# Optimization experiments

Hardware: AMD Instinct MI355X
Metric: run time of the kernel (lower is better)

The kernel has to match this reference:

```python
import jax, jax.numpy as jnp
import numpy as np

BS, NCAM, N, S = 2, 3, 64, 256


def setup_inputs() -> dict:
    key = jax.random.key(0)
    ks = jax.random.split(key, 7)
    # 2D projected points in pixel coordinates [0, image_size)
    points = jax.random.uniform(ks[0], (BS, NCAM, N, 2), dtype=jnp.float32) * S
    # blob params (per-point), realistic trained-model ranges
    sigmas = jax.random.uniform(ks[1], (BS, N), dtype=jnp.float32) * 0.05 + 0.02
    exponents = jax.random.uniform(ks[2], (BS, N), dtype=jnp.float32) * 0.5 + 0.75
    intensities = jax.random.uniform(ks[3], (BS, N), dtype=jnp.float32) * 0.5 + 0.5
    # per-camera scale factors, near 1
    camera_sigmas = jax.random.uniform(ks[4], (BS, NCAM), dtype=jnp.float32) * 0.2 + 0.9
    camera_exponents = jax.random.uniform(ks[5], (BS, NCAM), dtype=jnp.float32) * 0.2 + 0.9
    camera_intensities = jax.random.uniform(ks[6], (BS, NCAM), dtype=jnp.float32) * 0.2 + 0.9
    return {
        "points": points,
        "sigmas": sigmas,
        "exponents": exponents,
        "intensities": intensities,
        "camera_sigmas": camera_sigmas,
        "camera_exponents": camera_exponents,
        "camera_intensities": camera_intensities,
        "image_size": S,
    }


def reference(points, sigmas, exponents, intensities,
              camera_sigmas, camera_exponents, camera_intensities, image_size):
    """Faithful JAX port of render_points (render_mode='gaussians')."""
    bs, ncam, n = points.shape[0], points.shape[1], points.shape[2]
    s2 = image_size // 2
    # normalize pixel coords to [-1, 1] and flatten batch*cameras
    p = jnp.clip((points - s2) / s2, -1.0, 1.0).reshape(bs * ncam, n, 2)
    # per-point params scaled by per-camera factors; repeat_interleave(3,0)
    # on (bs,N) == broadcast over camera axis then flatten -> (bs*3, N, 1, 1)
    sig = (sigmas[:, None, :] * camera_sigmas[:, :, None]).reshape(bs * ncam, n, 1, 1)
    expn = (exponents[:, None, :] * camera_exponents[:, :, None]).reshape(bs * ncam, n, 1, 1)
    inten = (intensities[:, None, :] * camera_intensities[:, :, None]).reshape(bs * ncam, n, 1, 1)
    grid = jnp.linspace(-1.0, 1.0, image_size, dtype=jnp.float32)
    # m[y, x] = (grid[x], grid[y]); squared distance to each point
    dx = grid[None, None, None, :] - p[:, :, 0, None, None]   # (bs*3, N, 1, W)
    dy = grid[None, None, :, None] - p[:, :, 1, None, None]   # (bs*3, N, H, 1)
    dst = dx * dx + dy * dy                                   # (bs*3, N, H, W)
    blobs = jnp.exp(-((dst / (2.0 * sig * sig)) ** expn))      # (bs*3, N, H, W)
    masks = jnp.minimum(jnp.max(blobs * inten, axis=1), 1.0)   # amax over N, clamp(max=1)
    masks = masks.reshape(bs, ncam, image_size, image_size)
    blobs = blobs.reshape(bs, ncam, n, image_size, image_size)
    return masks, blobs
```

## Files before the change

kernel.cpp:

```cpp
#include <hip/hip_runtime.h>
#include <hip/hip_bf16.h>

constexpr int S_IMG = 256;
constexpr int NPT   = 64;
constexpr int BC    = 6;
constexpr int NCAM_ = 3;

__global__ __launch_bounds__(256) void render_blobs_kernel(
    const float* __restrict__ points,
    const float* __restrict__ sigmas,
    const float* __restrict__ exponents,
    const float* __restrict__ intensities,
    const float* __restrict__ cam_sig,
    const float* __restrict__ cam_exp,
    const float* __restrict__ cam_int,
    float* __restrict__ masks,
    float* __restrict__ blobs)
{
    const int blk = blockIdx.x;
    const int bc  = blk >> 7;
    const int y0  = (blk & 127) << 1;
    const int b   = bc / NCAM_;
    const int t   = threadIdx.x;

    __shared__ float spx[NPT], spy[NPT], sk[NPT], se[NPT], si[NPT];
    if (t < NPT) {
        const float inv = 1.0f / 128.0f;
        float px = points[(bc * NPT + t) * 2 + 0];
        float py = points[(bc * NPT + t) * 2 + 1];
        px = fminf(fmaxf((px - 128.0f) * inv, -1.0f), 1.0f);
        py = fminf(fmaxf((py - 128.0f) * inv, -1.0f), 1.0f);
        float sg = sigmas[b * NPT + t] * cam_sig[bc];
        spx[t] = px;
        spy[t] = py;
        sk[t]  = 1.0f / (2.0f * sg * sg);
        se[t]  = exponents[b * NPT + t] * cam_exp[bc];
        si[t]  = intensities[b * NPT + t] * cam_int[bc];
    }
    __syncthreads();

    const int lin = t << 1;
    const int y   = y0 + (lin >> 8);
    const int x   = lin & 255;

    const float step = 2.0f / 255.0f;
    const float gx0  = fmaf((float)x, step, -1.0f);
    const float gx1  = gx0 + step;
    const float gy   = fmaf((float)y, step, -1.0f);

    float m0 = 0.0f, m1 = 0.0f;
    float* bp = blobs + (size_t)bc * NPT * S_IMG * S_IMG + (size_t)y * S_IMG + x;
    const size_t nstride = (size_t)S_IMG * S_IMG;

    #pragma unroll 4
    for (int n = 0; n < NPT; ++n) {
        float dx0 = gx0 - spx[n];
        float dx1 = gx1 - spx[n];
        float dy  = gy  - spy[n];
        float dy2 = dy * dy;
        float u0  = fmaf(dx0, dx0, dy2) * sk[n];
        float u1  = fmaf(dx1, dx1, dy2) * sk[n];
        float e   = se[n];
        float v0 = exp2f(e * __log2f(u0));
        float v1 = exp2f(e * __log2f(u1));
        float b0 = exp2f(-1.4426950408889634f * v0);
        float b1 = exp2f(-1.4426950408889634f * v1);
        *reinterpret_cast<float2*>(bp + n * nstride) = make_float2(b0, b1);
        float it = si[n];
        m0 = fmaxf(m0, b0 * it);
        m1 = fmaxf(m1, b1 * it);
    }

    float2 mm = make_float2(fminf(m0, 1.0f), fminf(m1, 1.0f));
    *reinterpret_cast<float2*>(masks + (size_t)bc * S_IMG * S_IMG + (size_t)y * S_IMG + x) = mm;
}

extern "C" void kernel_launch(void* const* d_in, const int* in_sizes, int n_in,
                              void* d_out, int out_size, void* d_ws, size_t ws_size,
                              hipStream_t stream) {
    const float* points      = (const float*)d_in[0];
    const float* sigmas      = (const float*)d_in[1];
    const float* exponents   = (const float*)d_in[2];
    const float* intensities = (const float*)d_in[3];
    const float* cam_sig     = (const float*)d_in[4];
    const float* cam_exp     = (const float*)d_in[5];
    const float* cam_int     = (const float*)d_in[6];

    float* masks = (float*)d_out;
    float* blobs = (float*)d_out + (size_t)BC * S_IMG * S_IMG;

    dim3 grid(BC * (S_IMG / 2));
    dim3 block(256);
    render_blobs_kernel<<<grid, block, 0, stream>>>(
        points, sigmas, exponents, intensities, cam_sig, cam_exp, cam_int,
        masks, blobs);
}
```

Before: 24.26 us.

## Split blob writes and mask reduction into separate block roles with vec4 nontemporal stores

Blocks are split into two roles. Blob blocks each write one point's full 256x256 plane, so their float4 stores are contiguous and nontemporal. Separate mask blocks recompute all 64 blobs per pixel to take the max. This replaces the old scheme of 2-wide stores strided across 64 planes and aims to raise write efficiency on the dominant ~100MB blob output. The cost is that the mask path does a second full evaluation of the transcendental work.

```diff
diff --git a/kernel.cpp b/kernel.cpp
--- a/kernel.cpp
+++ b/kernel.cpp
@@ -1,12 +1,21 @@
 #include <hip/hip_runtime.h>
-#include <hip/hip_bf16.h>
 
 constexpr int S_IMG = 256;
 constexpr int NPT   = 64;
 constexpr int BC    = 6;
 constexpr int NCAM_ = 3;
+constexpr int NBLOB_BLOCKS = BC * NPT;
+constexpr int NMASK_BLOCKS = BC * (S_IMG / 2);
 
-__global__ __launch_bounds__(256) void render_blobs_kernel(
+typedef float vf4 __attribute__((ext_vector_type(4)));
+typedef float vf2 __attribute__((ext_vector_type(2)));
+
+__device__ __forceinline__ float blob_eval(float u, float e) {
+    float v = exp2f(e * __log2f(u));
+    return exp2f(-1.4426950408889634f * v);
+}
+
+__global__ __launch_bounds__(256) void render_all(
     const float* __restrict__ points,
     const float* __restrict__ sigmas,
     const float* __restrict__ exponents,
@@ -17,62 +26,100 @@
     float* __restrict__ masks,
     float* __restrict__ blobs)
 {
-    const int blk = blockIdx.x;
-    const int bc  = blk >> 7;
-    const int y0  = (blk & 127) << 1;
-    const int b   = bc / NCAM_;
-    const int t   = threadIdx.x;
+    const int   blk  = blockIdx.x;
+    const int   t    = threadIdx.x;
+    const float step = 2.0f / 255.0f;
 
-    __shared__ float spx[NPT], spy[NPT], sk[NPT], se[NPT], si[NPT];
-    if (t < NPT) {
-        const float inv = 1.0f / 128.0f;
-        float px = points[(bc * NPT + t) * 2 + 0];
-        float py = points[(bc * NPT + t) * 2 + 1];
-        px = fminf(fmaxf((px - 128.0f) * inv, -1.0f), 1.0f);
-        py = fminf(fmaxf((py - 128.0f) * inv, -1.0f), 1.0f);
-        float sg = sigmas[b * NPT + t] * cam_sig[bc];
-        spx[t] = px;
-        spy[t] = py;
-        sk[t]  = 1.0f / (2.0f * sg * sg);
-        se[t]  = exponents[b * NPT + t] * cam_exp[bc];
-        si[t]  = intensities[b * NPT + t] * cam_int[bc];
+    if (blk < NBLOB_BLOCKS) {
+        const int bc = blk >> 6;
+        const int n  = blk & 63;
+        const int b  = bc / NCAM_;
+
+        float px = points[blk * 2 + 0];
+        float py = points[blk * 2 + 1];
+        px = fminf(fmaxf((px - 128.0f) * (1.0f / 128.0f), -1.0f), 1.0f);
+        py = fminf(fmaxf((py - 128.0f) * (1.0f / 128.0f), -1.0f), 1.0f);
+        float sg = sigmas[b * NPT + n] * cam_sig[bc];
+        float k  = 1.0f / (2.0f * sg * sg);
+        float e  = exponents[b * NPT + n] * cam_exp[bc];
+
+        float* bp = blobs + ((size_t)blk << 16);
+
+        const int x0 = (t & 63) << 2;
+        const int ty = t >> 6;
+
+        float kdx2[4];
+        #pragma unroll
+        for (int j = 0; j < 4; ++j) {
+            float gx = fmaf((float)(x0 + j), step, -1.0f);
+            float dx = gx - px;
+            kdx2[j] = k * dx * dx;
+        }
+
+        #pragma unroll 2
+        for (int it = 0; it < 64; ++it) {
+            const int y  = (it << 2) | ty;
+            float gy  = fmaf((float)y, step, -1.0f);
+            float dyv = gy - py;
+            float kdy2 = k * dyv * dyv;
+            vf4 o;
+            o.x = blob_eval(kdx2[0] + kdy2, e);
+            o.y = blob_eval(kdx2[1] + kdy2, e);
+            o.z = blob_eval(kdx2[2] + kdy2, e);
+            o.w = blob_eval(kdx2[3] + kdy2, e);
+            __builtin_nontemporal_store(o, (vf4*)(bp + ((size_t)y << 8) + x0));
+        }
+    } else {
+        const int blk2 = blk - NBLOB_BLOCKS;
+        const int bc   = blk2 >> 7;
+        const int y0   = (blk2 & 127) << 1;
+        const int b    = bc / NCAM_;
+
+        __shared__ float spx[NPT], spy[NPT], sk[NPT], se[NPT], si[NPT];
+        if (t < NPT) {
+            float px = points[(bc * NPT + t) * 2 + 0];
+            float py = points[(bc * NPT + t) * 2 + 1];
+            px = fminf(fmaxf((px - 128.0f) * (1.0f / 128.0f), -1.0f), 1.0f);
+            py = fminf(fmaxf((py - 128.0f) * (1.0f / 128.0f), -1.0f), 1.0f);
+            float sg = sigmas[b * NPT + t] * cam_sig[bc];
+            spx[t] = px;
+            spy[t] = py;
+            sk[t]  = 1.0f / (2.0f * sg * sg);
+            se[t]  = exponents[b * NPT + t] * cam_exp[bc];
+            si[t]  = intensities[b * NPT + t] * cam_int[bc];
+        }
+        __syncthreads();
+
+        const int lin = t << 1;
+        const int y   = y0 + (lin >> 8);
+        const int x   = lin & 255;
+
+        const float gx0 = fmaf((float)x, step, -1.0f);
+        const float gx1 = gx0 + step;
+        const float gy  = fmaf((float)y, step, -1.0f);
+
+        float m0 = 0.0f, m1 = 0.0f;
+        #pragma unroll 4
+        for (int n = 0; n < NPT; ++n) {
+            float kk  = sk[n];
+            float dx0 = gx0 - spx[n];
+            float dx1 = gx1 - spx[n];
+            float dyv = gy  - spy[n];
+            float kdy2 = kk * dyv * dyv;
+            float e   = se[n];
+            float b0  = blob_eval(fmaf(kk * dx0, dx0, kdy2), e);
+            float b1  = blob_eval(fmaf(kk * dx1, dx1, kdy2), e);
+            float it  = si[n];
+            m0 = fmaxf(m0, b0 * it);
+            m1 = fmaxf(m1, b1 * it);
+        }
+
+        vf2 mm;
+        mm.x = fminf(m0, 1.0f);
+        mm.y = fminf(m1, 1.0f);
+        __builtin_nontemporal_store(
+            mm, (vf2*)(masks + ((size_t)bc << 16) + ((size_t)y << 8) + x));
     }
-    __syncthreads();
-
-    const int lin = t << 1;
-    const int y   = y0 + (lin >> 8);
-    const int x   = lin & 255;
-
-    const float step = 2.0f / 255.0f;
-    const float gx0  = fmaf((float)x, step, -1.0f);
-    const float gx1  = gx0 + step;
-    const float gy   = fmaf((float)y, step, -1.0f);
-
-    float m0 = 0.0f, m1 = 0.0f;
-    float* bp = blobs + (size_t)bc * NPT * S_IMG * S_IMG + (size_t)y * S_IMG + x;
-    const size_t nstride = (size_t)S_IMG * S_IMG;
-
-    #pragma unroll 4
-    for (int n = 0; n < NPT; ++n) {
-        float dx0 = gx0 - spx[n];
-        float dx1 = gx1 - spx[n];
-        float dy  = gy  - spy[n];
-        float dy2 = dy * dy;
-        float u0  = fmaf(dx0, dx0, dy2) * sk[n];
-        float u1  = fmaf(dx1, dx1, dy2) * sk[n];
-        float e   = se[n];
-        float v0 = exp2f(e * __log2f(u0));
-        float v1 = exp2f(e * __log2f(u1));
-        float b0 = exp2f(-1.4426950408889634f * v0);
-        float b1 = exp2f(-1.4426950408889634f * v1);
-        *reinterpret_cast<float2*>(bp + n * nstride) = make_float2(b0, b1);
-        float it = si[n];
-        m0 = fmaxf(m0, b0 * it);
-        m1 = fmaxf(m1, b1 * it);
-    }
-
-    float2 mm = make_float2(fminf(m0, 1.0f), fminf(m1, 1.0f));
-    *reinterpret_cast<float2*>(masks + (size_t)bc * S_IMG * S_IMG + (size_t)y * S_IMG + x) = mm;
 }
 
 extern "C" void kernel_launch(void* const* d_in, const int* in_sizes, int n_in,
@@ -89,9 +136,9 @@
     float* masks = (float*)d_out;
     float* blobs = (float*)d_out + (size_t)BC * S_IMG * S_IMG;
 
-    dim3 grid(BC * (S_IMG / 2));
+    dim3 grid(NBLOB_BLOCKS + NMASK_BLOCKS);
     dim3 block(256);
-    render_blobs_kernel<<<grid, block, 0, stream>>>(
+    render_all<<<grid, block, 0, stream>>>(
         points, sigmas, exponents, intensities, cam_sig, cam_exp, cam_int,
         masks, blobs);
 }
```

Measured after the change: 38.64 us. +59.3%, slower.

## Split point loop across two blocks and combine masks with atomicMax

Applied to the files above, without the earlier changes.

Each block now handles half of the 64 points for a pair of rows, so the grid doubles and each thread runs a shorter loop. Partial mask maxima are combined through integer atomicMax on the float bits, which is valid because the values are non-negative, after a memset zeroes the mask buffer. This adds parallelism and shortens per-thread latency, at the cost of an extra memset operation on the stream and atomic traffic on the masks. The distance computation is also refactored slightly, folding the scale factor into the fma.

```diff
diff --git a/kernel.cpp b/kernel.cpp
--- a/kernel.cpp
+++ b/kernel.cpp
@@ -1,12 +1,19 @@
 #include <hip/hip_runtime.h>
-#include <hip/hip_bf16.h>
 
 constexpr int S_IMG = 256;
 constexpr int NPT   = 64;
 constexpr int BC    = 6;
 constexpr int NCAM_ = 3;
+constexpr int NHALF = 32;
 
-__global__ __launch_bounds__(256) void render_blobs_kernel(
+typedef float vf2 __attribute__((ext_vector_type(2)));
+
+__device__ __forceinline__ float blob_eval(float u, float e) {
+    float v = exp2f(e * __log2f(u));
+    return exp2f(-1.4426950408889634f * v);
+}
+
+__global__ __launch_bounds__(256) void render_fused(
     const float* __restrict__ points,
     const float* __restrict__ sigmas,
     const float* __restrict__ exponents,
@@ -17,25 +24,27 @@
     float* __restrict__ masks,
     float* __restrict__ blobs)
 {
-    const int blk = blockIdx.x;
-    const int bc  = blk >> 7;
-    const int y0  = (blk & 127) << 1;
-    const int b   = bc / NCAM_;
-    const int t   = threadIdx.x;
+    const int blk      = blockIdx.x;
+    const int half     = blk & 1;
+    const int mask_idx = blk >> 1;
+    const int bc       = mask_idx >> 7;
+    const int y0       = (mask_idx & 127) << 1;
+    const int b        = bc / NCAM_;
+    const int t        = threadIdx.x;
 
-    __shared__ float spx[NPT], spy[NPT], sk[NPT], se[NPT], si[NPT];
-    if (t < NPT) {
-        const float inv = 1.0f / 128.0f;
-        float px = points[(bc * NPT + t) * 2 + 0];
-        float py = points[(bc * NPT + t) * 2 + 1];
-        px = fminf(fmaxf((px - 128.0f) * inv, -1.0f), 1.0f);
-        py = fminf(fmaxf((py - 128.0f) * inv, -1.0f), 1.0f);
-        float sg = sigmas[b * NPT + t] * cam_sig[bc];
+    __shared__ float spx[NHALF], spy[NHALF], sk[NHALF], se[NHALF], si[NHALF];
+    if (t < NHALF) {
+        const int n = (half << 5) + t;
+        float px = points[(bc * NPT + n) * 2 + 0];
+        float py = points[(bc * NPT + n) * 2 + 1];
+        px = fminf(fmaxf((px - 128.0f) * (1.0f / 128.0f), -1.0f), 1.0f);
+        py = fminf(fmaxf((py - 128.0f) * (1.0f / 128.0f), -1.0f), 1.0f);
+        float sg = sigmas[b * NPT + n] * cam_sig[bc];
         spx[t] = px;
         spy[t] = py;
         sk[t]  = 1.0f / (2.0f * sg * sg);
-        se[t]  = exponents[b * NPT + t] * cam_exp[bc];
-        si[t]  = intensities[b * NPT + t] * cam_int[bc];
+        se[t]  = exponents[b * NPT + n] * cam_exp[bc];
+        si[t]  = intensities[b * NPT + n] * cam_int[bc];
     }
     __syncthreads();
 
@@ -49,30 +58,33 @@
     const float gy   = fmaf((float)y, step, -1.0f);
 
     float m0 = 0.0f, m1 = 0.0f;
-    float* bp = blobs + (size_t)bc * NPT * S_IMG * S_IMG + (size_t)y * S_IMG + x;
+    float* bp = blobs + ((size_t)(bc * NPT + (half << 5)) << 16)
+                      + ((size_t)y << 8) + x;
     const size_t nstride = (size_t)S_IMG * S_IMG;
 
     #pragma unroll 4
-    for (int n = 0; n < NPT; ++n) {
-        float dx0 = gx0 - spx[n];
-        float dx1 = gx1 - spx[n];
-        float dy  = gy  - spy[n];
-        float dy2 = dy * dy;
-        float u0  = fmaf(dx0, dx0, dy2) * sk[n];
-        float u1  = fmaf(dx1, dx1, dy2) * sk[n];
-        float e   = se[n];
-        float v0 = exp2f(e * __log2f(u0));
-        float v1 = exp2f(e * __log2f(u1));
-        float b0 = exp2f(-1.4426950408889634f * v0);
-        float b1 = exp2f(-1.4426950408889634f * v1);
-        *reinterpret_cast<float2*>(bp + n * nstride) = make_float2(b0, b1);
+    for (int n = 0; n < NHALF; ++n) {
+        float kk   = sk[n];
+        float dx0  = gx0 - spx[n];
+        float dx1  = gx1 - spx[n];
+        float dyv  = gy  - spy[n];
+        float kdy2 = kk * dyv * dyv;
+        float e    = se[n];
+        float b0   = blob_eval(fmaf(kk * dx0, dx0, kdy2), e);
+        float b1   = blob_eval(fmaf(kk * dx1, dx1, kdy2), e);
+        vf2 o; o.x = b0; o.y = b1;
+        *reinterpret_cast<vf2*>(bp + n * nstride) = o;
         float it = si[n];
         m0 = fmaxf(m0, b0 * it);
         m1 = fmaxf(m1, b1 * it);
     }
 
-    float2 mm = make_float2(fminf(m0, 1.0f), fminf(m1, 1.0f));
-    *reinterpret_cast<float2*>(masks + (size_t)bc * S_IMG * S_IMG + (size_t)y * S_IMG + x) = mm;
+    m0 = fminf(m0, 1.0f);
+    m1 = fminf(m1, 1.0f);
+    unsigned int* mp = (unsigned int*)(masks + ((size_t)bc << 16)
+                                             + ((size_t)y << 8) + x);
+    atomicMax(mp + 0, __float_as_uint(m0));
+    atomicMax(mp + 1, __float_as_uint(m1));
 }
 
 extern "C" void kernel_launch(void* const* d_in, const int* in_sizes, int n_in,
@@ -89,9 +101,11 @@
     float* masks = (float*)d_out;
     float* blobs = (float*)d_out + (size_t)BC * S_IMG * S_IMG;
 
-    dim3 grid(BC * (S_IMG / 2));
+    hipMemsetAsync(masks, 0, (size_t)BC * S_IMG * S_IMG * sizeof(float), stream);
+
+    dim3 grid(BC * (S_IMG / 2) * 2);
     dim3 block(256);
-    render_blobs_kernel<<<grid, block, 0, stream>>>(
+    render_fused<<<grid, block, 0, stream>>>(
         points, sigmas, exponents, intensities, cam_sig, cam_exp, cam_int,
         masks, blobs);
 }
```

Result: slower. 29.67 us (+22.3%).
